# Kernel tuning notes

Hardware: AMD Instinct MI355X
Metric: run time of the kernel (lower is better)

The kernel has to match this reference:

```python
import jax, jax.numpy as jnp
import numpy as np
from jax import lax

NUM_CLASSES = 80
CONF_THRE = 0.01   # testconf in source
NMS_THRE = 0.2     # nmsthresh in source
N = 8400           # YOLOX anchors at 640x640: 80^2+40^2+20^2
IMG = 640.0


def setup_inputs() -> dict:
    key = jax.random.key(0)
    pred = jax.random.uniform(key, (N, 5 + NUM_CLASSES), dtype=jnp.float32)
    # scale cx,cy,w,h to pixel units so boxes are realistic
    pred = pred.at[:, :4].multiply(IMG)
    return {"prediction": pred}


def _pairwise_iou(boxes):
    # boxes: [N,4] in x1,y1,x2,y2
    area = (boxes[:, 2] - boxes[:, 0]) * (boxes[:, 3] - boxes[:, 1])  # [N]
    lt = jnp.maximum(boxes[:, None, :2], boxes[None, :, :2])  # [N,N,2]
    rb = jnp.minimum(boxes[:, None, 2:], boxes[None, :, 2:])  # [N,N,2]
    wh = jnp.clip(rb - lt, 0.0)
    inter = wh[..., 0] * wh[..., 1]
    return inter / (area[:, None] + area[None, :] - inter + 1e-9)


def reference(prediction):
    # ---- box corner decode (cx,cy,w,h -> x1,y1,x2,y2) ----
    cx, cy, w, h = prediction[:, 0], prediction[:, 1], prediction[:, 2], prediction[:, 3]
    boxes = jnp.stack([cx - w / 2, cy - h / 2, cx + w / 2, cy + h / 2], axis=1)

    # ---- per-class max ----
    cls_scores = prediction[:, 5:5 + NUM_CLASSES]
    class_conf = jnp.max(cls_scores, axis=1, keepdims=True)            # [N,1]
    class_pred = jnp.argmax(cls_scores, axis=1).astype(prediction.dtype)[:, None]

    obj = prediction[:, 4]
    valid = obj >= CONF_THRE                                            # conf mask

    # detections = [x1,y1,x2,y2, obj_conf, class_conf, class_pred]  -> [N,7]
    det = jnp.concatenate([boxes, obj[:, None], class_conf, class_pred], axis=1)

    # ---- class-agnostic greedy NMS on obj score (fixed-shape version) ----
    scores = jnp.where(valid, obj, -1.0)
    order = jnp.argsort(-scores)
    det_s = det[order]
    boxes_s = boxes[order]
    valid_s = valid[order]

    iou = _pairwise_iou(boxes_s)  # [N,N] ~282MB, dominant traffic
    idx = jnp.arange(N)

    def step(keep, inp):
        i, row, v = inp
        alive = keep[i] & v                      # only a kept valid box suppresses
        supp = alive & (row > NMS_THRE) & (idx > i)
        return keep & ~supp, None

    keep0 = jnp.ones((N,), dtype=bool)
    keep, _ = lax.scan(step, keep0, (idx, iou, valid_s))
    keep = keep & valid_s

    # suppressed / below-conf rows are zeroed (torch returns a ragged subset;
    # here we return the score-sorted, mask-zeroed fixed-shape equivalent)
    out = det_s * keep[:, None].astype(det_s.dtype)
    return out
```

## Files before the change

kernel.cpp:

```cpp
#include <hip/hip_runtime.h>
#include <stdint.h>

#define N_BOX 8400
#define NCLS 80
#define PSTRIDE 85
#define NW 132
#define NTILE 8778
#define ZROWI N_BOX
#define CONF_T 0.01f
#define NMS_T 0.2f

typedef unsigned long long u64;

#define OFF_DET     0
#define OFF_DIAGT   0
#define OFF_SUP1    67584
#define OFF_SUP2    135168
#define OFF_SUP3    202752
#define OFF_KEYS    268800
#define OFF_DETS    336000
#define OFF_BOXESS  604800
#define OFF_MASK    739200
#define OFF_KEEPW   9610656
#define OFF_VCNT    9611712

__device__ __forceinline__ unsigned fmap_desc(float f) {
    unsigned u = __float_as_uint(f);
    unsigned m = (u & 0x80000000u) ? ~u : (u | 0x80000000u);
    return ~m;
}

__device__ __forceinline__ u64 readlane64(u64 v, int lane) {
    unsigned lo = (unsigned)__builtin_amdgcn_readlane((int)(unsigned)v, lane);
    unsigned hi = (unsigned)__builtin_amdgcn_readlane((int)(unsigned)(v >> 32), lane);
    return ((u64)hi << 32) | lo;
}

__device__ __forceinline__ u64 shfl_xor64(u64 v, int m) {
    int lo = __shfl_xor((int)(unsigned)v, m);
    int hi = __shfl_xor((int)(unsigned)(v >> 32), m);
    return ((u64)(unsigned)hi << 32) | (unsigned)lo;
}

__device__ __forceinline__ u64 bittranspose64(u64 x, int lane) {
    const u64 P0 = 0x5555555555555555ull, P1 = 0x3333333333333333ull,
              P2 = 0x0F0F0F0F0F0F0F0Full, P3 = 0x00FF00FF00FF00FFull,
              P4 = 0x0000FFFF0000FFFFull, P5 = 0x00000000FFFFFFFFull;
#define TSTEP(s, p) do {                                                 \
        u64 y = shfl_xor64(x, s);                                        \
        x = (lane & (s)) ? ((x & ~(p)) | ((y & ~(p)) >> (s)))            \
                         : ((x & (p))  | ((y & (p))  << (s)));           \
    } while (0)
    TSTEP(1, P0); TSTEP(2, P1); TSTEP(4, P2);
    TSTEP(8, P3); TSTEP(16, P4); TSTEP(32, P5);
#undef TSTEP
    return x;
}

__device__ __forceinline__ u64 wmask(int w, int V) {
    int nb = V - (w << 6);
    if (nb <= 0) return 0ull;
    if (nb >= 64) return ~0ull;
    return (1ull << nb) - 1ull;
}

__device__ __forceinline__ void step_barrier() {
    asm volatile("s_waitcnt lgkmcnt(0)" ::: "memory");
    __builtin_amdgcn_s_barrier();
    asm volatile("" ::: "memory");
}

__global__ __launch_bounds__(256) void prep_k(const float* __restrict__ pred,
                                              float* __restrict__ det,
                                              u64* __restrict__ keys,
                                              u64* __restrict__ mask) {
    if (blockIdx.x == 0 && threadIdx.x < NW)
        mask[(size_t)ZROWI * NW + threadIdx.x] = 0ull;
    int gt = blockIdx.x * 256 + threadIdx.x;
    int i = gt >> 2, q = gt & 3;
    if (i >= N_BOX) return;
    const float* p = pred + (size_t)i * PSTRIDE;
    int cbase = q * 20;
    float best = p[5 + cbase];
    int arg = cbase;
    for (int c = 1; c < 20; ++c) {
        float v = p[5 + cbase + c];
        if (v > best) { best = v; arg = cbase + c; }
    }
    for (int d = 1; d < 4; d <<= 1) {
        float ob = __shfl_xor(best, d);
        int   oa = __shfl_xor(arg, d);
        if (ob > best || (ob == best && oa < arg)) { best = ob; arg = oa; }
    }
    if (q == 0) {
        float cx = p[0], cy = p[1], w = p[2], h = p[3], obj = p[4];
        float hw = __fmul_rn(w, 0.5f), hh = __fmul_rn(h, 0.5f);
        float x1 = __fsub_rn(cx, hw), y1 = __fsub_rn(cy, hh);
        float x2 = __fadd_rn(cx, hw), y2 = __fadd_rn(cy, hh);
        bool valid = (obj >= CONF_T);
        float score = valid ? obj : -1.0f;
        keys[i] = ((u64)fmap_desc(score) << 32) | (unsigned)i;
        float4* dr = (float4*)(det + (size_t)i * 8);
        dr[0] = make_float4(x1, y1, x2, y2);
        dr[1] = make_float4(obj, best, (float)arg, 0.0f);
    }
}

__global__ __launch_bounds__(256) void rank_k(const u64* __restrict__ keys,
                                              const float* __restrict__ det,
                                              float4* __restrict__ det_s,
                                              float4* __restrict__ boxes_s,
                                              int* __restrict__ vcount) {
    int t = threadIdx.x;
    int i = blockIdx.x * 32 + (t & 31);
    int s = t >> 5;
    u64 my = (i < N_BOX) ? keys[i] : ~0ull;
    int cnt = 0, cv = 0;
    int j0 = s * 1050, j1 = j0 + 1050;
    for (int j = j0; j < j1; j += 2) {
        ulonglong2 kk = *(const ulonglong2*)(keys + j);
        cnt += (kk.x < my) + (kk.y < my);
        cv  += ((long long)kk.x >= 0) + ((long long)kk.y >= 0);
    }
    __shared__ int sc[256], sv[256];
    sc[t] = cnt; sv[t] = cv;
    __syncthreads();
    if (t < 32) {
        int r = sc[t] + sc[t + 32] + sc[t + 64] + sc[t + 96]
              + sc[t + 128] + sc[t + 160] + sc[t + 192] + sc[t + 224];
        if (i < N_BOX) {
            const float4* dr = (const float4*)(det + (size_t)i * 8);
            float4 b0 = dr[0], b1 = dr[1];
            det_s[(size_t)r * 2]     = b0;
            det_s[(size_t)r * 2 + 1] = b1;
            boxes_s[r] = b0;
        }
        if (blockIdx.x == 0 && t == 0) {
            *vcount = sv[0] + sv[32] + sv[64] + sv[96]
                    + sv[128] + sv[160] + sv[192] + sv[224];
        }
    }
}

__global__ __launch_bounds__(64) void mask_k(const float4* __restrict__ boxes_s,
                                             u64* __restrict__ mask,
                                             u64* __restrict__ diagT,
                                             u64* __restrict__ sup1,
                                             u64* __restrict__ sup2,
                                             u64* __restrict__ sup3) {
    int tt = blockIdx.x, lane = threadIdx.x;
    int rb = (int)((2.0f * NW + 1.0f
                    - sqrtf((2.0f * NW + 1.0f) * (2.0f * NW + 1.0f) - 8.0f * (float)tt)) * 0.5f);
    while (rb > 0 && rb * NW - rb * (rb - 1) / 2 > tt) rb--;
    while ((rb + 1) * NW - (rb + 1) * rb / 2 <= tt) rb++;
    int cb = rb + (tt - (rb * NW - rb * (rb - 1) / 2));

    __shared__ float4 cB[64];
    __shared__ float  cA[64];
    int c0 = cb * 64 + lane;
    float4 b = (c0 < N_BOX) ? boxes_s[c0] : make_float4(0.f, 0.f, 0.f, 0.f);
    cB[lane] = b;
    cA[lane] = __fmul_rn(__fsub_rn(b.z, b.x), __fsub_rn(b.w, b.y));
    __syncthreads();
    int r = rb * 64 + lane;
    bool inb = (r < N_BOX);
    float4 rx = boxes_s[inb ? r : (N_BOX - 1)];
    float ra = __fmul_rn(__fsub_rn(rx.z, rx.x), __fsub_rn(rx.w, rx.y));
    u64 bits = 0ull;
    int cbase = cb * 64;
    for (int j = 0; j < 64; ++j) {
        int c = cbase + j;
        if (c >= N_BOX || c <= r) continue;
        float4 cx4 = cB[j];
        float ltx = fmaxf(rx.x, cx4.x), lty = fmaxf(rx.y, cx4.y);
        float rbx = fminf(rx.z, cx4.z), rby = fminf(rx.w, cx4.w);
        float wx = fmaxf(__fsub_rn(rbx, ltx), 0.0f);
        float wy = fmaxf(__fsub_rn(rby, lty), 0.0f);
        float inter = __fmul_rn(wx, wy);
        float denom = __fadd_rn(__fsub_rn(__fadd_rn(ra, cA[j]), inter), 1e-9f);
        float iou = __fdiv_rn(inter, denom);
        if (iou > NMS_T) bits |= (1ull << j);
    }
    if (inb) mask[(size_t)r * NW + cb] = bits;
    int d = cb - rb;
    if (d <= 3) {
        u64 tb = bittranspose64(bits, lane);
        size_t idx = (size_t)cb * 64 + lane;
        if (d == 0)      diagT[idx] = tb;
        else if (d == 1) sup1[idx]  = tb;
        else if (d == 2) sup2[idx]  = tb;
        else             sup3[idx]  = tb;
    }
}

__global__ __launch_bounds__(128, 1) void scan_k(const u64* __restrict__ mask,
                                                 const u64* __restrict__ diagT,
                                                 const u64* __restrict__ sup1,
                                                 const u64* __restrict__ sup2,
                                                 const u64* __restrict__ sup3,
                                                 const int* __restrict__ vcount,
                                                 u64* __restrict__ keepw) {
    __shared__ u64 remvP[NW + 2];
    __shared__ u64 Lbuf[NW];
    int tid = threadIdx.x, lane = tid & 63, wv = tid >> 6;
    int V = *vcount;
    for (int i = tid; i < NW + 2; i += 128) remvP[i] = 0ull;
    __syncthreads();

    if (wv == 0) {
        u64 A1 = 0ull, A2 = 0ull, A3 = 0ull;
        u64 d0P, s1P, s2P, s3P, d0Q, s1Q, s2Q, s3Q;

#define TL(S, kk) do {                                                   \
        int t_ = (kk) < NW ? (kk) : (NW - 1);                            \
        size_t ix_ = (size_t)t_ * 64 + lane;                             \
        d0##S = diagT[ix_]; s1##S = sup1[ix_];                           \
        s2##S = sup2[ix_];  s3##S = sup3[ix_];                           \
    } while (0)

#define STEP0(kk, S) do {                                                \
        int k_ = (kk);                                                   \
        u64 cur_ = remvP[k_];                                            \
        cur_ |= __ballot((s1##S & A1) != 0ull);                          \
        cur_ |= __ballot((s2##S & A2) != 0ull);                          \
        cur_ |= __ballot((s3##S & A3) != 0ull);                          \
        u64 m_ = wmask(k_, V);                                           \
        u64 ns_ = (~cur_) & m_;                                          \
        u64 L_ = 0ull;                                                   \
        while (ns_) {                                                    \
            int b_ = __builtin_ctzll(ns_);                               \
            L_ |= 1ull << b_;                                            \
            u64 sup_ = __ballot((int)((d0##S >> b_) & 1ull));            \
            ns_ &= ~sup_;                                                \
            ns_ &= ~(1ull << b_);                                        \
        }                                                                \
        if (lane == 0) { Lbuf[k_] = L_; keepw[k_] = L_; }                \
        A3 = A2; A2 = A1; A1 = L_;                                       \
        TL(S, k_ + 2);                                                   \
        step_barrier();                                                  \
    } while (0)

        TL(P, 0);
        TL(Q, 1);
        for (int c = 0; c < NW; c += 2) {
            STEP0(c + 0, P);
            STEP0(c + 1, Q);
        }
#undef STEP0
#undef TL
    } else {
        int tw = (lane < 4) ? (128 + lane) : 131;
        u64 Ra = 0ull, Rb = 0ull, Rc = 0ull;
        u64 Pa0=0,Pa1=0,Pa2=0,Pa3=0,Pa4=0,Pa5=0,Pa6=0,Pa7=0;
        u64 Pb0=0,Pb1=0,Pb2=0,Pb3=0,Pb4=0,Pb5=0,Pb6=0,Pb7=0;
        u64 Pc0=0,Pc1=0,Pc2=0,Pc3=0,Pc4=0,Pc5=0,Pc6=0,Pc7=0;
        u64 Qa0=0,Qa1=0,Qa2=0,Qa3=0,Qa4=0,Qa5=0,Qa6=0,Qa7=0;
        u64 Qb0=0,Qb1=0,Qb2=0,Qb3=0,Qb4=0,Qb5=0,Qb6=0,Qb7=0;
        u64 Qc0=0,Qc1=0,Qc2=0,Qc3=0,Qc4=0,Qc5=0,Qc6=0,Qc7=0;

#define CONS(S) do {                                                     \
        Ra |= ((S##a0|S##a1)|(S##a2|S##a3))|((S##a4|S##a5)|(S##a6|S##a7));\
        Rb |= ((S##b0|S##b1)|(S##b2|S##b3))|((S##b4|S##b5)|(S##b6|S##b7));\
        Rc |= ((S##c0|S##c1)|(S##c2|S##c3))|((S##c4|S##c5)|(S##c6|S##c7));\
    } while (0)

#define LROW(S, i) do {                                                  \
        size_t ri_ = rem_ ? (size_t)(rbase_ + __builtin_ctzll(rem_))     \
                          : (size_t)ZROWI;                               \
        rem_ &= rem_ - 1ull;                                             \
        const u64* rp_ = mask + ri_ * NW;                                \
        ulonglong2 v_ = *(const ulonglong2*)(rp_ + 2 * lane);            \
        S##a##i = v_.x; S##b##i = v_.y; S##c##i = rp_[tw];               \
    } while (0)

#define STEP1(jj, S) do {                                                \
        int j_ = (jj);                                                   \
        CONS(S);                                  \
        int w_ = j_ + 1;                                                 \
        u64 rw_ = (w_ < 128) ? ((w_ & 1) ? Rb : Ra) : Rc;                \
        int sl_ = (w_ < 128) ? (w_ >> 1) : (w_ - 128);                   \
        u64 pv_ = readlane64(rw_, sl_);                                  \
        if (lane == 0) remvP[w_] = pv_;                                  \
        u64 Lp_ = Lbuf[j_ >= 1 ? j_ - 1 : 0];                            \
        if (j_ < 1) Lp_ = 0ull;                                          \
        int rbase_ = (j_ - 1) << 6;                                      \
        u64 rem_ = Lp_;                                                  \
        LROW(S, 0); LROW(S, 1); LROW(S, 2); LROW(S, 3);                  \
        LROW(S, 4); LROW(S, 5); LROW(S, 6); LROW(S, 7);                  \
        while (rem_) {                             \
            u64 xa_ = 0, xb_ = 0, xc_ = 0;                               \
            for (int q_ = 0; q_ < 16; ++q_) {                            \
                size_t ri_ = rem_ ? (size_t)(rbase_ + __builtin_ctzll(rem_)) \
                                  : (size_t)ZROWI;                       \
                rem_ &= rem_ - 1ull;                                     \
                const u64* rp_ = mask + ri_ * NW;                        \
                ulonglong2 v_ = *(const ulonglong2*)(rp_ + 2 * lane);    \
                xa_ |= v_.x; xb_ |= v_.y; xc_ |= rp_[tw];                \
            }                                                            \
            Ra |= xa_; Rb |= xb_; Rc |= xc_;                             \
        }                                                                \
        step_barrier();                                                  \
    } while (0)

        for (int c = 0; c < NW; c += 2) {
            STEP1(c + 0, P);
            STEP1(c + 1, Q);
        }
#undef STEP1
#undef LROW
#undef CONS
    }
}

__global__ __launch_bounds__(256) void out_k(const float* __restrict__ det_s,
                                             const u64* __restrict__ keepw,
                                             float* __restrict__ out) {
    int e = blockIdx.x * 256 + threadIdx.x;
    if (e >= N_BOX * 7) return;
    int r = e / 7, c = e - r * 7;
    bool k = (keepw[r >> 6] >> (r & 63)) & 1ull;
    out[e] = k ? det_s[r * 8 + c] : 0.0f;
}

extern "C" void kernel_launch(void* const* d_in, const int* in_sizes, int n_in,
                              void* d_out, int out_size, void* d_ws, size_t ws_size,
                              hipStream_t stream) {
    const float* pred = (const float*)d_in[0];
    char* ws = (char*)d_ws;
    float*  det     = (float*) (ws + OFF_DET);
    u64*    diagT   = (u64*)   (ws + OFF_DIAGT);
    u64*    sup1    = (u64*)   (ws + OFF_SUP1);
    u64*    sup2    = (u64*)   (ws + OFF_SUP2);
    u64*    sup3    = (u64*)   (ws + OFF_SUP3);
    u64*    keys    = (u64*)   (ws + OFF_KEYS);
    float*  det_s   = (float*) (ws + OFF_DETS);
    float4* boxes_s = (float4*)(ws + OFF_BOXESS);
    u64*    mask    = (u64*)   (ws + OFF_MASK);
    u64*    keepw   = (u64*)   (ws + OFF_KEEPW);
    int*    vcount  = (int*)   (ws + OFF_VCNT);

    prep_k<<<132, 256, 0, stream>>>(pred, det, keys, mask);
    rank_k<<<264, 256, 0, stream>>>(keys, det, (float4*)det_s, boxes_s, vcount);
    mask_k<<<NTILE, 64, 0, stream>>>(boxes_s, mask, diagT, sup1, sup2, sup3);
    scan_k<<<1, 128, 0, stream>>>(mask, diagT, sup1, sup2, sup3, vcount, keepw);
    out_k <<<(N_BOX * 7 + 255) / 256, 256, 0, stream>>>(det_s, keepw, (float*)d_out);
}
```

Baseline: 153.8 us.

## Stage suppression rows into LDS asynchronously and shrink rank keys to 32-bit

The scan kernel's helper wavefront now issues global_load_lds copies of up to 16 mask rows (plus tails) into double-buffered LDS slots. It folds them into the shared remv words two steps later, so the serial dependence chain is pipelined rather than stalling on register loads each step. Rows beyond 16 fall back to direct global loads. The rank kernel uses 32-bit keys, with explicit index tie-breaking, and reads them as uint4, halving key traffic. The change adds vmcnt/lgkmcnt sequencing and a longer lag before suppression bits take effect, which is a correctness risk if the timing assumptions are off.

Measured after the change: 238.0 us. 54.7% more time.

```diff
diff --git a/kernel.cpp b/kernel.cpp
--- a/kernel.cpp
+++ b/kernel.cpp
@@ -28,12 +28,6 @@
     unsigned u = __float_as_uint(f);
     unsigned m = (u & 0x80000000u) ? ~u : (u | 0x80000000u);
     return ~m;
-}
-
-__device__ __forceinline__ u64 readlane64(u64 v, int lane) {
-    unsigned lo = (unsigned)__builtin_amdgcn_readlane((int)(unsigned)v, lane);
-    unsigned hi = (unsigned)__builtin_amdgcn_readlane((int)(unsigned)(v >> 32), lane);
-    return ((u64)hi << 32) | lo;
 }
 
 __device__ __forceinline__ u64 shfl_xor64(u64 v, int m) {
@@ -64,15 +58,34 @@
     return (1ull << nb) - 1ull;
 }
 
+__device__ __forceinline__ int selbit(u64 v, int k) {
+    int idx = 0;
+    int c = __popcll(v & 0xFFFFFFFFull);
+    if (k >= c) { k -= c; idx += 32; v >>= 32; }
+    unsigned lo = (unsigned)v;
+    c = __popc(lo & 0xFFFFu); if (k >= c) { k -= c; idx += 16; lo >>= 16; }
+    c = __popc(lo & 0xFFu);   if (k >= c) { k -= c; idx += 8;  lo >>= 8;  }
+    c = __popc(lo & 0xFu);    if (k >= c) { k -= c; idx += 4;  lo >>= 4;  }
+    c = __popc(lo & 0x3u);    if (k >= c) { k -= c; idx += 2;  lo >>= 2;  }
+    c = lo & 1u;              if (k >= c) { idx += 1; }
+    return idx;
+}
+
 __device__ __forceinline__ void step_barrier() {
     asm volatile("s_waitcnt lgkmcnt(0)" ::: "memory");
     __builtin_amdgcn_s_barrier();
     asm volatile("" ::: "memory");
 }
 
+__device__ __forceinline__ void gload16(const void* gsrc, void* lds_dst) {
+    __builtin_amdgcn_global_load_lds(
+        (const __attribute__((address_space(1))) void*)gsrc,
+        (__attribute__((address_space(3))) void*)lds_dst, 16, 0, 0);
+}
+
 __global__ __launch_bounds__(256) void prep_k(const float* __restrict__ pred,
                                               float* __restrict__ det,
-                                              u64* __restrict__ keys,
+                                              unsigned* __restrict__ keys,
                                               u64* __restrict__ mask) {
     if (blockIdx.x == 0 && threadIdx.x < NW)
         mask[(size_t)ZROWI * NW + threadIdx.x] = 0ull;
@@ -99,14 +112,14 @@
         float x2 = __fadd_rn(cx, hw), y2 = __fadd_rn(cy, hh);
         bool valid = (obj >= CONF_T);
         float score = valid ? obj : -1.0f;
-        keys[i] = ((u64)fmap_desc(score) << 32) | (unsigned)i;
+        keys[i] = fmap_desc(score);
         float4* dr = (float4*)(det + (size_t)i * 8);
         dr[0] = make_float4(x1, y1, x2, y2);
         dr[1] = make_float4(obj, best, (float)arg, 0.0f);
     }
 }
 
-__global__ __launch_bounds__(256) void rank_k(const u64* __restrict__ keys,
+__global__ __launch_bounds__(256) void rank_k(const unsigned* __restrict__ keys,
                                               const float* __restrict__ det,
                                               float4* __restrict__ det_s,
                                               float4* __restrict__ boxes_s,
@@ -114,13 +127,21 @@
     int t = threadIdx.x;
     int i = blockIdx.x * 32 + (t & 31);
     int s = t >> 5;
-    u64 my = (i < N_BOX) ? keys[i] : ~0ull;
+    unsigned my = (i < N_BOX) ? keys[i] : 0xFFFFFFFFu;
     int cnt = 0, cv = 0;
-    int j0 = s * 1050, j1 = j0 + 1050;
-    for (int j = j0; j < j1; j += 2) {
-        ulonglong2 kk = *(const ulonglong2*)(keys + j);
-        cnt += (kk.x < my) + (kk.y < my);
-        cv  += ((long long)kk.x >= 0) + ((long long)kk.y >= 0);
+    int j0 = s * 1050;
+    for (int j = j0; j < j0 + 1048; j += 4) {
+        uint4 k4 = *(const uint4*)(keys + j);
+        cnt += (k4.x < my) + (k4.y < my) + (k4.z < my) + (k4.w < my);
+        cnt += (k4.x == my && j     < i) + (k4.y == my && j + 1 < i)
+             + (k4.z == my && j + 2 < i) + (k4.w == my && j + 3 < i);
+        cv  += ((int)k4.x >= 0) + ((int)k4.y >= 0) + ((int)k4.z >= 0) + ((int)k4.w >= 0);
+    }
+    {
+        unsigned ka = keys[j0 + 1048], kb = keys[j0 + 1049];
+        cnt += (ka < my) + (kb < my)
+             + (ka == my && j0 + 1048 < i) + (kb == my && j0 + 1049 < i);
+        cv  += ((int)ka >= 0) + ((int)kb >= 0);
     }
     __shared__ int sc[256], sv[256];
     sc[t] = cnt; sv[t] = cv;
@@ -200,27 +221,27 @@
                                                  const u64* __restrict__ sup3,
                                                  const int* __restrict__ vcount,
                                                  u64* __restrict__ keepw) {
-    __shared__ u64 remvP[NW + 2];
+    __shared__ __align__(16) u64 rows[2][16][128];
+    __shared__ __align__(16) u64 tails[2][128];
+    __shared__ u64 remvW[NW];
     __shared__ u64 Lbuf[NW];
     int tid = threadIdx.x, lane = tid & 63, wv = tid >> 6;
     int V = *vcount;
-    for (int i = tid; i < NW + 2; i += 128) remvP[i] = 0ull;
+    for (int i = tid; i < NW; i += 128) { remvW[i] = 0ull; Lbuf[i] = 0ull; }
     __syncthreads();
 
     if (wv == 0) {
         u64 A1 = 0ull, A2 = 0ull, A3 = 0ull;
         u64 d0P, s1P, s2P, s3P, d0Q, s1Q, s2Q, s3Q;
-
 #define TL(S, kk) do {                                                   \
         int t_ = (kk) < NW ? (kk) : (NW - 1);                            \
         size_t ix_ = (size_t)t_ * 64 + lane;                             \
         d0##S = diagT[ix_]; s1##S = sup1[ix_];                           \
         s2##S = sup2[ix_];  s3##S = sup3[ix_];                           \
     } while (0)
-
 #define STEP0(kk, S) do {                                                \
         int k_ = (kk);                                                   \
-        u64 cur_ = remvP[k_];                                            \
+        u64 cur_ = remvW[k_];                                            \
         cur_ |= __ballot((s1##S & A1) != 0ull);                          \
         cur_ |= __ballot((s2##S & A2) != 0ull);                          \
         cur_ |= __ballot((s3##S & A3) != 0ull);                          \
@@ -239,7 +260,6 @@
         TL(S, k_ + 2);                                                   \
         step_barrier();                                                  \
     } while (0)
-
         TL(P, 0);
         TL(Q, 1);
         for (int c = 0; c < NW; c += 2) {
@@ -249,66 +269,69 @@
 #undef STEP0
 #undef TL
     } else {
-        int tw = (lane < 4) ? (128 + lane) : 131;
-        u64 Ra = 0ull, Rb = 0ull, Rc = 0ull;
-        u64 Pa0=0,Pa1=0,Pa2=0,Pa3=0,Pa4=0,Pa5=0,Pa6=0,Pa7=0;
-        u64 Pb0=0,Pb1=0,Pb2=0,Pb3=0,Pb4=0,Pb5=0,Pb6=0,Pb7=0;
-        u64 Pc0=0,Pc1=0,Pc2=0,Pc3=0,Pc4=0,Pc5=0,Pc6=0,Pc7=0;
-        u64 Qa0=0,Qa1=0,Qa2=0,Qa3=0,Qa4=0,Qa5=0,Qa6=0,Qa7=0;
-        u64 Qb0=0,Qb1=0,Qb2=0,Qb3=0,Qb4=0,Qb5=0,Qb6=0,Qb7=0;
-        u64 Qc0=0,Qc1=0,Qc2=0,Qc3=0,Qc4=0,Qc5=0,Qc6=0,Qc7=0;
-
-#define CONS(S) do {                                                     \
-        Ra |= ((S##a0|S##a1)|(S##a2|S##a3))|((S##a4|S##a5)|(S##a6|S##a7));\
-        Rb |= ((S##b0|S##b1)|(S##b2|S##b3))|((S##b4|S##b5)|(S##b6|S##b7));\
-        Rc |= ((S##c0|S##c1)|(S##c2|S##c3))|((S##c4|S##c5)|(S##c6|S##c7));\
-    } while (0)
-
-#define LROW(S, i) do {                                                  \
-        size_t ri_ = rem_ ? (size_t)(rbase_ + __builtin_ctzll(rem_))     \
-                          : (size_t)ZROWI;                               \
-        rem_ &= rem_ - 1ull;                                             \
-        const u64* rp_ = mask + ri_ * NW;                                \
-        ulonglong2 v_ = *(const ulonglong2*)(rp_ + 2 * lane);            \
-        S##a##i = v_.x; S##b##i = v_.y; S##c##i = rp_[tw];               \
-    } while (0)
-
-#define STEP1(jj, S) do {                                                \
-        int j_ = (jj);                                                   \
-        CONS(S);                                  \
-        int w_ = j_ + 1;                                                 \
-        u64 rw_ = (w_ < 128) ? ((w_ & 1) ? Rb : Ra) : Rc;                \
-        int sl_ = (w_ < 128) ? (w_ >> 1) : (w_ - 128);                   \
-        u64 pv_ = readlane64(rw_, sl_);                                  \
-        if (lane == 0) remvP[w_] = pv_;                                  \
-        u64 Lp_ = Lbuf[j_ >= 1 ? j_ - 1 : 0];                            \
-        if (j_ < 1) Lp_ = 0ull;                                          \
-        int rbase_ = (j_ - 1) << 6;                                      \
-        u64 rem_ = Lp_;                                                  \
-        LROW(S, 0); LROW(S, 1); LROW(S, 2); LROW(S, 3);                  \
-        LROW(S, 4); LROW(S, 5); LROW(S, 6); LROW(S, 7);                  \
-        while (rem_) {                             \
-            u64 xa_ = 0, xb_ = 0, xc_ = 0;                               \
-            for (int q_ = 0; q_ < 16; ++q_) {                            \
-                size_t ri_ = rem_ ? (size_t)(rbase_ + __builtin_ctzll(rem_)) \
-                                  : (size_t)ZROWI;                       \
-                rem_ &= rem_ - 1ull;                                     \
-                const u64* rp_ = mask + ri_ * NW;                        \
-                ulonglong2 v_ = *(const ulonglong2*)(rp_ + 2 * lane);    \
-                xa_ |= v_.x; xb_ |= v_.y; xc_ |= rp_[tw];                \
-            }                                                            \
-            Ra |= xa_; Rb |= xb_; Rc |= xc_;                             \
-        }                                                                \
-        step_barrier();                                                  \
-    } while (0)
-
-        for (int c = 0; c < NW; c += 2) {
-            STEP1(c + 0, P);
-            STEP1(c + 1, Q);
+        for (int j = 0; j < NW; ++j) {
+            int slot = j & 1;
+            if (j >= 2) {
+                asm volatile("s_waitcnt vmcnt(17)" ::: "memory");
+                __builtin_amdgcn_sched_barrier(0);
+                u64 Lc = Lbuf[j - 3 >= 0 ? j - 3 : 0];
+                if (j < 3) Lc = 0ull;
+                int nr = __popcll(Lc); nr = nr < 16 ? nr : 16;
+                u64 a0 = 0ull, a1 = 0ull, at = 0ull;
+                int tix = (lane & 3);
+                for (int r = 0; r < nr; ++r) {
+                    ulonglong2 v = *(const ulonglong2*)&rows[slot][r][2 * lane];
+                    a0 |= v.x; a1 |= v.y;
+                    at |= tails[slot][4 * r + 2 * (tix >> 1) + (tix & 1)];
+                }
+                remvW[2 * lane]     |= a0;
+                remvW[2 * lane + 1] |= a1;
+                if (lane < 4) remvW[128 + lane] |= at;
+                asm volatile("s_waitcnt lgkmcnt(0)" ::: "memory");
+                __builtin_amdgcn_sched_barrier(0);
+            }
+            u64 Lp = (j >= 1) ? Lbuf[j - 1] : 0ull;
+            int rbase = (j - 1) << 6;
+            int cntL = __popcll(Lp);
+            if (cntL > 16) {
+                u64 rem = Lp;
+                for (int s = 0; s < 16; ++s) rem &= rem - 1ull;
+                int tw = (lane < 4) ? (128 + lane) : 131;
+                u64 xa = 0ull, xb = 0ull, xc = 0ull;
+                while (rem) {
+                    size_t ri = (size_t)(rbase + __builtin_ctzll(rem));
+                    rem &= rem - 1ull;
+                    const u64* rp = mask + ri * NW;
+                    ulonglong2 v = *(const ulonglong2*)(rp + 2 * lane);
+                    xa |= v.x; xb |= v.y; xc |= rp[tw];
+                }
+                remvW[2 * lane]     |= xa;
+                remvW[2 * lane + 1] |= xb;
+                if (lane < 4) remvW[128 + lane] |= xc;
+            }
+            {
+                u64 rem = Lp;
+                int i0, i1, i2, i3, i4, i5, i6, i7, i8, i9, i10, i11, i12, i13, i14, i15;
+#define NXT(dst) do { dst = rem ? (rbase + __builtin_ctzll(rem)) : ZROWI;  \
+                      rem &= rem - 1ull; } while (0)
+                NXT(i0); NXT(i1); NXT(i2); NXT(i3);
+                NXT(i4); NXT(i5); NXT(i6); NXT(i7);
+                NXT(i8); NXT(i9); NXT(i10); NXT(i11);
+                NXT(i12); NXT(i13); NXT(i14); NXT(i15);
+#undef NXT
+#define GL(rr, ii) gload16(mask + (size_t)(ii) * NW + 2 * lane, &rows[slot][rr][0])
+                GL(0, i0);  GL(1, i1);  GL(2, i2);  GL(3, i3);
+                GL(4, i4);  GL(5, i5);  GL(6, i6);  GL(7, i7);
+                GL(8, i8);  GL(9, i9);  GL(10, i10); GL(11, i11);
+                GL(12, i12); GL(13, i13); GL(14, i14); GL(15, i15);
+#undef GL
+                int rsel = lane >> 1;
+                int ri = (rsel < cntL && rsel < 16) ? (rbase + selbit(Lp, rsel)) : ZROWI;
+                const u64* tsrc = mask + (size_t)ri * NW + 128 + 2 * (lane & 1);
+                gload16(tsrc, &tails[slot][0]);
+            }
+            step_barrier();
         }
-#undef STEP1
-#undef LROW
-#undef CONS
     }
 }
 
@@ -327,17 +350,17 @@
                               hipStream_t stream) {
     const float* pred = (const float*)d_in[0];
     char* ws = (char*)d_ws;
-    float*  det     = (float*) (ws + OFF_DET);
-    u64*    diagT   = (u64*)   (ws + OFF_DIAGT);
-    u64*    sup1    = (u64*)   (ws + OFF_SUP1);
-    u64*    sup2    = (u64*)   (ws + OFF_SUP2);
-    u64*    sup3    = (u64*)   (ws + OFF_SUP3);
-    u64*    keys    = (u64*)   (ws + OFF_KEYS);
-    float*  det_s   = (float*) (ws + OFF_DETS);
-    float4* boxes_s = (float4*)(ws + OFF_BOXESS);
-    u64*    mask    = (u64*)   (ws + OFF_MASK);
-    u64*    keepw   = (u64*)   (ws + OFF_KEEPW);
-    int*    vcount  = (int*)   (ws + OFF_VCNT);
+    float*    det     = (float*)   (ws + OFF_DET);
+    u64*      diagT   = (u64*)     (ws + OFF_DIAGT);
+    u64*      sup1    = (u64*)     (ws + OFF_SUP1);
+    u64*      sup2    = (u64*)     (ws + OFF_SUP2);
+    u64*      sup3    = (u64*)     (ws + OFF_SUP3);
+    unsigned* keys    = (unsigned*)(ws + OFF_KEYS);
+    float*    det_s   = (float*)   (ws + OFF_DETS);
+    float4*   boxes_s = (float4*)  (ws + OFF_BOXESS);
+    u64*      mask    = (u64*)     (ws + OFF_MASK);
+    u64*      keepw   = (u64*)     (ws + OFF_KEEPW);
+    int*      vcount  = (int*)     (ws + OFF_VCNT);
 
     prep_k<<<132, 256, 0, stream>>>(pred, det, keys, mask);
     rank_k<<<264, 256, 0, stream>>>(keys, det, (float4*)det_s, boxes_s, vcount);
```

## Split scan row-OR work across two waves and shrink rank keys to 32-bit

Applied to the files above, without the earlier changes.

The sequential NMS scan kernel now runs three wavefronts instead of two. The two helper waves each take half of the kept-bit word from the previous step and OR the suppression rows for that half into their own shared buffer. The lead wave combines both buffers, which halves the serial row-load chain per step. Separately, the rank keys drop from 64 bits to 32, with index tie-breaking computed explicitly in the compare loop, which halves key traffic but adds extra compares.

New measurement: 155.0 us. No clear change (+0.8%).

```diff
diff --git a/kernel.cpp b/kernel.cpp
--- a/kernel.cpp
+++ b/kernel.cpp
@@ -72,7 +72,7 @@
 
 __global__ __launch_bounds__(256) void prep_k(const float* __restrict__ pred,
                                               float* __restrict__ det,
-                                              u64* __restrict__ keys,
+                                              unsigned* __restrict__ keys,
                                               u64* __restrict__ mask) {
     if (blockIdx.x == 0 && threadIdx.x < NW)
         mask[(size_t)ZROWI * NW + threadIdx.x] = 0ull;
@@ -99,14 +99,14 @@
         float x2 = __fadd_rn(cx, hw), y2 = __fadd_rn(cy, hh);
         bool valid = (obj >= CONF_T);
         float score = valid ? obj : -1.0f;
-        keys[i] = ((u64)fmap_desc(score) << 32) | (unsigned)i;
+        keys[i] = fmap_desc(score);
         float4* dr = (float4*)(det + (size_t)i * 8);
         dr[0] = make_float4(x1, y1, x2, y2);
         dr[1] = make_float4(obj, best, (float)arg, 0.0f);
     }
 }
 
-__global__ __launch_bounds__(256) void rank_k(const u64* __restrict__ keys,
+__global__ __launch_bounds__(256) void rank_k(const unsigned* __restrict__ keys,
                                               const float* __restrict__ det,
                                               float4* __restrict__ det_s,
                                               float4* __restrict__ boxes_s,
@@ -114,13 +114,16 @@
     int t = threadIdx.x;
     int i = blockIdx.x * 32 + (t & 31);
     int s = t >> 5;
-    u64 my = (i < N_BOX) ? keys[i] : ~0ull;
+    unsigned my = (i < N_BOX) ? keys[i] : 0xFFFFFFFFu;
     int cnt = 0, cv = 0;
-    int j0 = s * 1050, j1 = j0 + 1050;
-    for (int j = j0; j < j1; j += 2) {
-        ulonglong2 kk = *(const ulonglong2*)(keys + j);
-        cnt += (kk.x < my) + (kk.y < my);
-        cv  += ((long long)kk.x >= 0) + ((long long)kk.y >= 0);
+    int j0 = s * 1056;
+    int jend = (s == 7) ? N_BOX : (j0 + 1056);
+    for (int j = j0; j < jend; j += 4) {
+        uint4 k4 = *(const uint4*)(keys + j);
+        cnt += (k4.x < my) + (k4.y < my) + (k4.z < my) + (k4.w < my);
+        cnt += (k4.x == my && j     < i) + (k4.y == my && j + 1 < i)
+             + (k4.z == my && j + 2 < i) + (k4.w == my && j + 3 < i);
+        cv  += ((int)k4.x >= 0) + ((int)k4.y >= 0) + ((int)k4.z >= 0) + ((int)k4.w >= 0);
     }
     __shared__ int sc[256], sv[256];
     sc[t] = cnt; sv[t] = cv;
@@ -193,34 +196,33 @@
     }
 }
 
-__global__ __launch_bounds__(128, 1) void scan_k(const u64* __restrict__ mask,
+__global__ __launch_bounds__(192, 1) void scan_k(const u64* __restrict__ mask,
                                                  const u64* __restrict__ diagT,
                                                  const u64* __restrict__ sup1,
                                                  const u64* __restrict__ sup2,
                                                  const u64* __restrict__ sup3,
                                                  const int* __restrict__ vcount,
                                                  u64* __restrict__ keepw) {
-    __shared__ u64 remvP[NW + 2];
+    __shared__ u64 remvP1[NW + 2];
+    __shared__ u64 remvP2[NW + 2];
     __shared__ u64 Lbuf[NW];
     int tid = threadIdx.x, lane = tid & 63, wv = tid >> 6;
     int V = *vcount;
-    for (int i = tid; i < NW + 2; i += 128) remvP[i] = 0ull;
+    for (int i = tid; i < NW + 2; i += 192) { remvP1[i] = 0ull; remvP2[i] = 0ull; }
     __syncthreads();
 
     if (wv == 0) {
         u64 A1 = 0ull, A2 = 0ull, A3 = 0ull;
         u64 d0P, s1P, s2P, s3P, d0Q, s1Q, s2Q, s3Q;
-
 #define TL(S, kk) do {                                                   \
         int t_ = (kk) < NW ? (kk) : (NW - 1);                            \
         size_t ix_ = (size_t)t_ * 64 + lane;                             \
         d0##S = diagT[ix_]; s1##S = sup1[ix_];                           \
         s2##S = sup2[ix_];  s3##S = sup3[ix_];                           \
     } while (0)
-
 #define STEP0(kk, S) do {                                                \
         int k_ = (kk);                                                   \
-        u64 cur_ = remvP[k_];                                            \
+        u64 cur_ = remvP1[k_] | remvP2[k_];                              \
         cur_ |= __ballot((s1##S & A1) != 0ull);                          \
         cur_ |= __ballot((s2##S & A2) != 0ull);                          \
         cur_ |= __ballot((s3##S & A3) != 0ull);                          \
@@ -239,7 +241,6 @@
         TL(S, k_ + 2);                                                   \
         step_barrier();                                                  \
     } while (0)
-
         TL(P, 0);
         TL(Q, 1);
         for (int c = 0; c < NW; c += 2) {
@@ -249,25 +250,23 @@
 #undef STEP0
 #undef TL
     } else {
+        int half = wv - 1;
+        u64* myP = half ? remvP2 : remvP1;
         int tw = (lane < 4) ? (128 + lane) : 131;
         u64 Ra = 0ull, Rb = 0ull, Rc = 0ull;
-        u64 Pa0=0,Pa1=0,Pa2=0,Pa3=0,Pa4=0,Pa5=0,Pa6=0,Pa7=0;
-        u64 Pb0=0,Pb1=0,Pb2=0,Pb3=0,Pb4=0,Pb5=0,Pb6=0,Pb7=0;
-        u64 Pc0=0,Pc1=0,Pc2=0,Pc3=0,Pc4=0,Pc5=0,Pc6=0,Pc7=0;
-        u64 Qa0=0,Qa1=0,Qa2=0,Qa3=0,Qa4=0,Qa5=0,Qa6=0,Qa7=0;
-        u64 Qb0=0,Qb1=0,Qb2=0,Qb3=0,Qb4=0,Qb5=0,Qb6=0,Qb7=0;
-        u64 Qc0=0,Qc1=0,Qc2=0,Qc3=0,Qc4=0,Qc5=0,Qc6=0,Qc7=0;
+        u64 Pa0=0,Pa1=0,Pa2=0,Pa3=0, Pb0=0,Pb1=0,Pb2=0,Pb3=0, Pc0=0,Pc1=0,Pc2=0,Pc3=0;
+        u64 Qa0=0,Qa1=0,Qa2=0,Qa3=0, Qb0=0,Qb1=0,Qb2=0,Qb3=0, Qc0=0,Qc1=0,Qc2=0,Qc3=0;
 
 #define CONS(S) do {                                                     \
-        Ra |= ((S##a0|S##a1)|(S##a2|S##a3))|((S##a4|S##a5)|(S##a6|S##a7));\
-        Rb |= ((S##b0|S##b1)|(S##b2|S##b3))|((S##b4|S##b5)|(S##b6|S##b7));\
-        Rc |= ((S##c0|S##c1)|(S##c2|S##c3))|((S##c4|S##c5)|(S##c6|S##c7));\
+        Ra |= (S##a0 | S##a1) | (S##a2 | S##a3);                         \
+        Rb |= (S##b0 | S##b1) | (S##b2 | S##b3);                         \
+        Rc |= (S##c0 | S##c1) | (S##c2 | S##c3);                         \
     } while (0)
 
 #define LROW(S, i) do {                                                  \
-        size_t ri_ = rem_ ? (size_t)(rbase_ + __builtin_ctzll(rem_))     \
+        size_t ri_ = rem_ ? (size_t)(rbase_ + __builtin_ctz(rem_))       \
                           : (size_t)ZROWI;                               \
-        rem_ &= rem_ - 1ull;                                             \
+        rem_ &= rem_ - 1u;                                               \
         const u64* rp_ = mask + ri_ * NW;                                \
         ulonglong2 v_ = *(const ulonglong2*)(rp_ + 2 * lane);            \
         S##a##i = v_.x; S##b##i = v_.y; S##c##i = rp_[tw];               \
@@ -280,19 +279,18 @@
         u64 rw_ = (w_ < 128) ? ((w_ & 1) ? Rb : Ra) : Rc;                \
         int sl_ = (w_ < 128) ? (w_ >> 1) : (w_ - 128);                   \
         u64 pv_ = readlane64(rw_, sl_);                                  \
-        if (lane == 0) remvP[w_] = pv_;                                  \
-        u64 Lp_ = Lbuf[j_ >= 1 ? j_ - 1 : 0];                            \
-        if (j_ < 1) Lp_ = 0ull;                                          \
-        int rbase_ = (j_ - 1) << 6;                                      \
-        u64 rem_ = Lp_;                                                  \
+        if (lane == 0) myP[w_] = pv_;                                    \
+        u64 Lfull_ = (j_ >= 1) ? Lbuf[j_ - 1] : 0ull;                    \
+        unsigned rem_ = half ? (unsigned)(Lfull_ >> 32)                  \
+                             : (unsigned)Lfull_;                         \
+        int rbase_ = ((j_ - 1) << 6) + 32 * half;                        \
         LROW(S, 0); LROW(S, 1); LROW(S, 2); LROW(S, 3);                  \
-        LROW(S, 4); LROW(S, 5); LROW(S, 6); LROW(S, 7);                  \
-        while (rem_) {                             \
+        while (rem_) {                              \
             u64 xa_ = 0, xb_ = 0, xc_ = 0;                               \
-            for (int q_ = 0; q_ < 16; ++q_) {                            \
-                size_t ri_ = rem_ ? (size_t)(rbase_ + __builtin_ctzll(rem_)) \
+            for (int q_ = 0; q_ < 8; ++q_) {                             \
+                size_t ri_ = rem_ ? (size_t)(rbase_ + __builtin_ctz(rem_)) \
                                   : (size_t)ZROWI;                       \
-                rem_ &= rem_ - 1ull;                                     \
+                rem_ &= rem_ - 1u;                                       \
                 const u64* rp_ = mask + ri_ * NW;                        \
                 ulonglong2 v_ = *(const ulonglong2*)(rp_ + 2 * lane);    \
                 xa_ |= v_.x; xb_ |= v_.y; xc_ |= rp_[tw];                \
@@ -327,21 +325,21 @@
                               hipStream_t stream) {
     const float* pred = (const float*)d_in[0];
     char* ws = (char*)d_ws;
-    float*  det     = (float*) (ws + OFF_DET);
-    u64*    diagT   = (u64*)   (ws + OFF_DIAGT);
-    u64*    sup1    = (u64*)   (ws + OFF_SUP1);
-    u64*    sup2    = (u64*)   (ws + OFF_SUP2);
-    u64*    sup3    = (u64*)   (ws + OFF_SUP3);
-    u64*    keys    = (u64*)   (ws + OFF_KEYS);
-    float*  det_s   = (float*) (ws + OFF_DETS);
-    float4* boxes_s = (float4*)(ws + OFF_BOXESS);
-    u64*    mask    = (u64*)   (ws + OFF_MASK);
-    u64*    keepw   = (u64*)   (ws + OFF_KEEPW);
-    int*    vcount  = (int*)   (ws + OFF_VCNT);
+    float*    det     = (float*)   (ws + OFF_DET);
+    u64*      diagT   = (u64*)     (ws + OFF_DIAGT);
+    u64*      sup1    = (u64*)     (ws + OFF_SUP1);
+    u64*      sup2    = (u64*)     (ws + OFF_SUP2);
+    u64*      sup3    = (u64*)     (ws + OFF_SUP3);
+    unsigned* keys    = (unsigned*)(ws + OFF_KEYS);
+    float*    det_s   = (float*)   (ws + OFF_DETS);
+    float4*   boxes_s = (float4*)  (ws + OFF_BOXESS);
+    u64*      mask    = (u64*)     (ws + OFF_MASK);
+    u64*      keepw   = (u64*)     (ws + OFF_KEEPW);
+    int*      vcount  = (int*)     (ws + OFF_VCNT);
 
     prep_k<<<132, 256, 0, stream>>>(pred, det, keys, mask);
     rank_k<<<264, 256, 0, stream>>>(keys, det, (float4*)det_s, boxes_s, vcount);
     mask_k<<<NTILE, 64, 0, stream>>>(boxes_s, mask, diagT, sup1, sup2, sup3);
-    scan_k<<<1, 128, 0, stream>>>(mask, diagT, sup1, sup2, sup3, vcount, keepw);
+    scan_k<<<1, 192, 0, stream>>>(mask, diagT, sup1, sup2, sup3, vcount, keepw);
     out_k <<<(N_BOX * 7 + 255) / 256, 256, 0, stream>>>(det_s, keepw, (float*)d_out);
 }
```
